# Kernel optimization log

Measured on AMD Instinct MI355X. Metric: run time of the kernel, lower is better.

Reference implementation:

```python
import jax, jax.numpy as jnp
import numpy as np
import math

D_MODEL = 1024
N_HEADS = 16
D_KV = 64
INNER = N_HEADS * D_KV
D_FF = 4096
NUM_BUCKETS = 32
MAX_DIST = 128
EPS = 1e-6
B, S = 2, 1024


def _t5_layernorm(x, w):
    # T5 RMSNorm: no mean subtraction, no bias
    var = jnp.mean(x * x, axis=-1, keepdims=True)
    return x * jax.lax.rsqrt(var + EPS) * w


def _relative_position_bucket(relative_position):
    # bidirectional (encoder) variant of T5 bucketing
    num_buckets = NUM_BUCKETS // 2
    rel_buckets = (relative_position > 0).astype(jnp.int32) * num_buckets
    rp = jnp.abs(relative_position)
    max_exact = num_buckets // 2
    is_small = rp < max_exact
    rp_large = max_exact + (
        jnp.log(rp.astype(jnp.float32) / max_exact)
        / math.log(MAX_DIST / max_exact)
        * (num_buckets - max_exact)
    ).astype(jnp.int32)
    rp_large = jnp.minimum(rp_large, num_buckets - 1)
    return rel_buckets + jnp.where(is_small, rp, rp_large)


def setup_inputs() -> dict:
    key = jax.random.key(0)
    ks = jax.random.split(key, 8)
    sc = 0.02
    return {
        "hidden_states": jax.random.normal(ks[0], (B, S, D_MODEL), jnp.float32),
        "ln1_w": jnp.ones((D_MODEL,), jnp.float32),
        "wq": jax.random.normal(ks[1], (INNER, D_MODEL), jnp.float32) * sc,
        "wk": jax.random.normal(ks[2], (INNER, D_MODEL), jnp.float32) * sc,
        "wv": jax.random.normal(ks[3], (INNER, D_MODEL), jnp.float32) * sc,
        "wo": jax.random.normal(ks[4], (D_MODEL, INNER), jnp.float32) * sc,
        "rel_bias": jax.random.normal(ks[5], (NUM_BUCKETS, N_HEADS), jnp.float32) * sc,
        "ln2_w": jnp.ones((D_MODEL,), jnp.float32),
        "wi": jax.random.normal(ks[6], (D_FF, D_MODEL), jnp.float32) * sc,
        "wo_ff": jax.random.normal(ks[7], (D_MODEL, D_FF), jnp.float32) * sc,
    }


def reference(hidden_states, ln1_w, wq, wk, wv, wo, rel_bias, ln2_w, wi, wo_ff):
    b, s, _ = hidden_states.shape
    # --- self-attention with relative position bias (T5: no 1/sqrt(d) scale) ---
    x = _t5_layernorm(hidden_states, ln1_w)
    q = (x @ wq.T).reshape(b, s, N_HEADS, D_KV).transpose(0, 2, 1, 3)  # [b,h,s,d]
    k = (x @ wk.T).reshape(b, s, N_HEADS, D_KV).transpose(0, 2, 1, 3)
    v = (x @ wv.T).reshape(b, s, N_HEADS, D_KV).transpose(0, 2, 1, 3)
    pos = jnp.arange(s)
    buckets = _relative_position_bucket(pos[None, :] - pos[:, None])  # [s,s]
    bias = rel_bias[buckets].transpose(2, 0, 1)[None]  # [1,h,s,s]
    scores = jnp.einsum('bhqd,bhkd->bhqk', q, k) + bias
    attn = jax.nn.softmax(scores, axis=-1)
    ctx = jnp.einsum('bhqk,bhkd->bhqd', attn, v)
    ctx = ctx.transpose(0, 2, 1, 3).reshape(b, s, INNER)
    h = hidden_states + ctx @ wo.T
    # --- FFN (ReLU dense) with pre-norm and residual ---
    y = _t5_layernorm(h, ln2_w)
    ff = jax.nn.relu(y @ wi.T) @ wo_ff.T
    return h + ff
```

## Files before the change

### kernel.cpp

```cpp
#include <hip/hip_runtime.h>
#include <hip/hip_bf16.h>
#include <math.h>


typedef __bf16 bf16_t;
typedef __attribute__((ext_vector_type(8))) __bf16 bf16x8;
typedef __attribute__((ext_vector_type(4))) __bf16 bf16x4;
typedef __attribute__((ext_vector_type(4))) float floatx4;

#define GLOBAL_AS(p) ((const __attribute__((address_space(1))) void*)(p))
#define LDS_AS(p)    ((__attribute__((address_space(3))) void*)(p))

__global__ __launch_bounds__(256) void convert_w_kernel(
    const float* __restrict__ wq, const float* __restrict__ wk,
    const float* __restrict__ wv, const float* __restrict__ wo,
    const float* __restrict__ wi, const float* __restrict__ woff,
    bf16_t* __restrict__ wqkv_b, bf16_t* __restrict__ wo_b,
    bf16_t* __restrict__ wi_b, bf16_t* __restrict__ woff_b) {
  size_t idx = ((size_t)blockIdx.x * 256 + threadIdx.x) * 8;
  const float* src;
  bf16_t* dst;
  size_t off;
  if (idx < 3145728) {
    size_t sec = idx >> 20;
    src = sec == 0 ? wq : (sec == 1 ? wk : wv);
    dst = wqkv_b + (sec << 20);
    off = idx & 1048575;
  } else if (idx < 4194304) {
    src = wo; dst = wo_b; off = idx - 3145728;
  } else if (idx < 8388608) {
    src = wi; dst = wi_b; off = idx - 4194304;
  } else {
    src = woff; dst = woff_b; off = idx - 8388608;
  }
  float4 a = *(const float4*)(src + off);
  float4 b = *(const float4*)(src + off + 4);
  bf16x8 o;
  o[0] = (bf16_t)a.x; o[1] = (bf16_t)a.y; o[2] = (bf16_t)a.z; o[3] = (bf16_t)a.w;
  o[4] = (bf16_t)b.x; o[5] = (bf16_t)b.y; o[6] = (bf16_t)b.z; o[7] = (bf16_t)b.w;
  *(bf16x8*)(dst + off) = o;
}

__global__ void bias_table_kernel(const float* __restrict__ rel_bias,
                                  float* __restrict__ table) {
  int idx = blockIdx.x * 256 + threadIdx.x;
  int h = idx >> 11;
  int dpos = idx & 2047;
  int delta = dpos - 1023;
  if (delta > 1023) delta = 1023;
  int side = (delta > 0) ? 16 : 0;
  int rp = (delta < 0) ? -delta : delta;
  int bucket;
  if (rp < 8) {
    bucket = side + rp;
  } else {
    float t3 = (logf((float)rp * 0.125f) / 2.7725887f) * 8.0f;
    int v = 8 + (int)t3;
    if (v > 15) v = 15;
    bucket = side + v;
  }
  table[idx] = rel_bias[bucket * 16 + h];
}

__global__ __launch_bounds__(256) void rmsnorm_kernel(
    const float* __restrict__ X, const float* __restrict__ w,
    bf16_t* __restrict__ Y) {
  const int D = 1024;
  int row = blockIdx.x;
  int t = threadIdx.x;
  float4 v = ((const float4*)(X + (size_t)row * D))[t];
  float f[4] = {v.x, v.y, v.z, v.w};
  float s = 0.f;
#pragma unroll
  for (int j = 0; j < 4; ++j) s += f[j] * f[j];
#pragma unroll
  for (int off = 32; off > 0; off >>= 1) s += __shfl_down(s, off);
  __shared__ float red[4];
  int lane = t & 63, wave = t >> 6;
  if (lane == 0) red[wave] = s;
  __syncthreads();
  float tot = red[0] + red[1] + red[2] + red[3];
  float scale = rsqrtf(tot * (1.0f / D) + 1e-6f);
  float4 wv4 = ((const float4*)w)[t];
  bf16x4 o;
  o[0] = (bf16_t)(f[0] * scale * wv4.x);
  o[1] = (bf16_t)(f[1] * scale * wv4.y);
  o[2] = (bf16_t)(f[2] * scale * wv4.z);
  o[3] = (bf16_t)(f[3] * scale * wv4.w);
  *(bf16x4*)(Y + (size_t)row * D + t * 4) = o;
}

template <int TBM, bool WF32, int OP>
__global__ __launch_bounds__(256, 2) void gemm_bt(
    const bf16_t* __restrict__ A, const void* __restrict__ W0,
    const void* __restrict__ W1, const void* __restrict__ W2,
    bf16_t* __restrict__ C, int M, int K_total, int klen, int N,
    int wsel_cols) {
  constexpr int MFRAG = TBM / 32;
  constexpr int ACH = TBM / 64;
  __shared__ bf16_t As[TBM * 32];
  __shared__ bf16_t Bs[128 * 32];

  const int tid = threadIdx.x;
  const int lane = tid & 63;
  const int wv = tid >> 6;
  const int wm = wv & 1;
  const int wn = wv >> 1;
  const int lr = lane & 15;
  const int lq = lane >> 4;

  const size_t row0 = (size_t)blockIdx.x * TBM;
  const size_t col0 = (size_t)blockIdx.y * 128;
  const int k0 = blockIdx.z * klen;

  const void* Ws = W0;
  size_t wc0 = col0;
  if ((int)col0 >= wsel_cols) {
    if ((int)col0 < 2 * wsel_cols) { Ws = W1; wc0 = col0 - wsel_cols; }
    else { Ws = W2; wc0 = col0 - 2 * (size_t)wsel_cols; }
  }

  const bf16_t* Abase = A + row0 * K_total;
  bf16_t* Cs = C + (size_t)blockIdx.z * M * N;

  floatx4 acc[MFRAG][4] = {};

  for (int kt = k0; kt < k0 + klen; kt += 32) {
#pragma unroll
    for (int i = 0; i < ACH; ++i) {
      int chunk = i * 256 + tid;
      int r = chunk >> 2;
      int kc = (chunk & 3) << 3;
      __builtin_amdgcn_global_load_lds(
          GLOBAL_AS(Abase + (size_t)r * K_total + kt + kc),
          LDS_AS(As + (size_t)(i * 256 + wv * 64) * 8), 16, 0, 0);
    }
    if constexpr (WF32) {
      const float* Wbase = (const float*)Ws + wc0 * K_total;
#pragma unroll
      for (int i = 0; i < 2; ++i) {
        int chunk = i * 256 + tid;
        int r = chunk >> 2;
        int kc = (chunk & 3) << 3;
        const float* p = Wbase + (size_t)r * K_total + kt + kc;
        float4 f0 = *(const float4*)p;
        float4 f1v = *(const float4*)(p + 4);
        bf16x8 o;
        o[0] = (bf16_t)f0.x; o[1] = (bf16_t)f0.y;
        o[2] = (bf16_t)f0.z; o[3] = (bf16_t)f0.w;
        o[4] = (bf16_t)f1v.x; o[5] = (bf16_t)f1v.y;
        o[6] = (bf16_t)f1v.z; o[7] = (bf16_t)f1v.w;
        *(bf16x8*)(Bs + chunk * 8) = o;
      }
    } else {
      const bf16_t* Wbase = (const bf16_t*)Ws + wc0 * K_total;
#pragma unroll
      for (int i = 0; i < 2; ++i) {
        int chunk = i * 256 + tid;
        int r = chunk >> 2;
        int kc = (chunk & 3) << 3;
        __builtin_amdgcn_global_load_lds(
            GLOBAL_AS(Wbase + (size_t)r * K_total + kt + kc),
            LDS_AS(Bs + (size_t)(i * 256 + wv * 64) * 8), 16, 0, 0);
      }
    }
    __syncthreads();

    bf16x8 af[MFRAG], bfr[4];
#pragma unroll
    for (int mi = 0; mi < MFRAG; ++mi)
      af[mi] = *(const bf16x8*)(As + (wm * (TBM / 2) + mi * 16 + lr) * 32 + lq * 8);
#pragma unroll
    for (int nj = 0; nj < 4; ++nj)
      bfr[nj] = *(const bf16x8*)(Bs + (wn * 64 + nj * 16 + lr) * 32 + lq * 8);

#pragma unroll
    for (int mi = 0; mi < MFRAG; ++mi)
#pragma unroll
      for (int nj = 0; nj < 4; ++nj)
        acc[mi][nj] = __builtin_amdgcn_mfma_f32_16x16x32_bf16(
            af[mi], bfr[nj], acc[mi][nj], 0, 0, 0);
    __syncthreads();
  }

#pragma unroll
  for (int mi = 0; mi < MFRAG; ++mi) {
#pragma unroll
    for (int nj = 0; nj < 4; ++nj) {
      size_t r = row0 + wm * (TBM / 2) + mi * 16 + lq * 4;
      size_t c = col0 + wn * 64 + nj * 16 + lr;
#pragma unroll
      for (int t = 0; t < 4; ++t) {
        float v = acc[mi][nj][t];
        if (OP == 2) v = v > 0.f ? v : 0.f;
        Cs[(r + t) * N + c] = (bf16_t)v;
      }
    }
  }
}

__global__ __launch_bounds__(256) void transpose_v_kernel(
    const bf16_t* __restrict__ QKV, bf16_t* __restrict__ VT) {
  __shared__ bf16_t T[64 * 65];
  const int s0 = blockIdx.x * 64;
  const int h = blockIdx.y;
  const int b = blockIdx.z;
  const int tid = threadIdx.x;

  const bf16_t* Vh = QKV + ((size_t)b * 1024) * 3072 + 2048 + h * 64;
#pragma unroll
  for (int i = 0; i < 2; ++i) {
    int c = i * 256 + tid;
    int r = c >> 3;
    int d8 = (c & 7) * 8;
    bf16x8 v = *(const bf16x8*)(Vh + (size_t)(s0 + r) * 3072 + d8);
#pragma unroll
    for (int j = 0; j < 8; ++j) T[r * 65 + d8 + j] = v[j];
  }
  __syncthreads();

  bf16_t* Og = VT + ((size_t)b * 16 + h) * 64 * 1024;
#pragma unroll
  for (int i = 0; i < 2; ++i) {
    int c = i * 256 + tid;
    int d = c >> 3;
    int s8 = (c & 7) * 8;
    bf16x8 o;
#pragma unroll
    for (int j = 0; j < 8; ++j) o[j] = T[(s8 + j) * 65 + d];
    *(bf16x8*)(Og + (size_t)d * 1024 + s0 + s8) = o;
  }
}

__device__ __forceinline__ void attn_stage(const bf16_t* Kh, const bf16_t* Vg,
                                           int k0, bf16_t* Ksb, bf16_t* Vtb,
                                           int tid, int wv) {
  const int l16 = tid & 15;
  const int lo8 = ((tid & 63) >> 4) * 8;
#pragma unroll
  for (int i = 0; i < 2; ++i) {
    int bi = wv * 2 + i;
    int g = bi >> 1, c = bi & 1;
    __builtin_amdgcn_global_load_lds(
        GLOBAL_AS(Kh + (size_t)(k0 + g * 16 + l16) * 3072 + c * 32 + lo8),
        LDS_AS(Ksb + bi * 512), 16, 0, 0);
    __builtin_amdgcn_global_load_lds(
        GLOBAL_AS(Vg + (size_t)(g * 16 + l16) * 1024 + k0 + c * 32 + lo8),
        LDS_AS(Vtb + bi * 512), 16, 0, 0);
  }
}

__global__ __launch_bounds__(256) void attn_kernel(
    const bf16_t* __restrict__ QKV, const bf16_t* __restrict__ VT,
    const float* __restrict__ bias_table, bf16_t* __restrict__ O) {
  const int qt = blockIdx.x;
  const int h = blockIdx.y;
  const int b = blockIdx.z;
  const int tid = threadIdx.x;
  const int lane = tid & 63;
  const int wv = tid >> 6;
  const int lr = lane & 15;
  const int lq = lane >> 4;

  __shared__ bf16_t Ks[2][4096];
  __shared__ bf16_t Vt[2][4096];
  __shared__ bf16_t Ps[4][1024];

  const bf16_t* Qh = QKV + (size_t)b * 1024 * 3072 + h * 64;
  const bf16_t* Kh = Qh + 1024;
  const bf16_t* Vg = VT + ((size_t)b * 16 + h) * 64 * 1024;
  bf16_t* Oh = O + (size_t)b * 1024 * 1024 + h * 64;

  const int q0w = qt * 64 + wv * 16;
  const int myq = q0w + lr;

  bf16x8 qf[2];
#pragma unroll
  for (int c = 0; c < 2; ++c)
    qf[c] = *(const bf16x8*)(Qh + (size_t)(q0w + lr) * 3072 + c * 32 + lq * 8);

  float l_loc = 0.f;
  floatx4 o_acc[4];
#pragma unroll
  for (int i = 0; i < 4; ++i) o_acc[i] = (floatx4){0.f, 0.f, 0.f, 0.f};

  const float* btab = bias_table + h * 2048 + 1023 - myq;

  attn_stage(Kh, Vg, 0, Ks[0], Vt[0], tid, wv);
  __syncthreads();

  for (int kt = 0; kt < 16; ++kt) {
    const int k0 = kt * 64;
    if (kt < 15)
      attn_stage(Kh, Vg, k0 + 64, Ks[(kt + 1) & 1], Vt[(kt + 1) & 1], tid, wv);
    const bf16_t* Ksb = Ks[kt & 1];
    const bf16_t* Vtb = Vt[kt & 1];

    floatx4 s_acc[4];
#pragma unroll
    for (int g = 0; g < 4; ++g) {
      floatx4 a = (floatx4){0.f, 0.f, 0.f, 0.f};
#pragma unroll
      for (int c = 0; c < 2; ++c) {
        bf16x8 kf = *(const bf16x8*)(Ksb + (g * 2 + c) * 512 + lane * 8);
        a = __builtin_amdgcn_mfma_f32_16x16x32_bf16(kf, qf[c], a, 0, 0, 0);
      }
      s_acc[g] = a;
    }

#pragma unroll
    for (int g = 0; g < 4; ++g) {
      bf16x4 pb;
#pragma unroll
      for (int t = 0; t < 4; ++t) {
        int key = k0 + g * 16 + lq * 4 + t;
        float p = __expf(s_acc[g][t] + btab[key] - 32.0f);
        l_loc += p;
        pb[t] = (bf16_t)p;
      }
      int c = g >> 1;
      int dst = c * 512 + (((g & 1) * 2 + (lq >> 1)) * 16 + lr) * 8 + (lq & 1) * 4;
      *(bf16x4*)(&Ps[wv][dst]) = pb;
    }

    asm volatile("s_waitcnt lgkmcnt(0)" ::: "memory");

    bf16x8 pf[2];
#pragma unroll
    for (int c = 0; c < 2; ++c)
      pf[c] = *(const bf16x8*)(&Ps[wv][c * 512 + lane * 8]);

#pragma unroll
    for (int g = 0; g < 4; ++g) {
#pragma unroll
      for (int c = 0; c < 2; ++c) {
        bf16x8 vf = *(const bf16x8*)(Vtb + (g * 2 + c) * 512 + lane * 8);
        o_acc[g] = __builtin_amdgcn_mfma_f32_16x16x32_bf16(pf[c], vf, o_acc[g], 0, 0, 0);
      }
    }
    __syncthreads();
  }

  l_loc += __shfl_xor(l_loc, 16);
  l_loc += __shfl_xor(l_loc, 32);
  float inv = 1.f / l_loc;

  float invt[4];
#pragma unroll
  for (int t = 0; t < 4; ++t) invt[t] = __shfl(inv, lq * 4 + t);

#pragma unroll
  for (int g = 0; g < 4; ++g) {
#pragma unroll
    for (int t = 0; t < 4; ++t) {
      int qg = q0w + lq * 4 + t;
      int d = g * 16 + lr;
      Oh[(size_t)qg * 1024 + d] = (bf16_t)(o_acc[g][t] * invt[t]);
    }
  }
}

__global__ __launch_bounds__(256) void reduce_rms_kernel(
    const bf16_t* __restrict__ part, int splits, const float* __restrict__ hs,
    const float* __restrict__ ln2w, bf16_t* __restrict__ hbuf,
    bf16_t* __restrict__ y) {
  const size_t SLICE = (size_t)2048 * 1024;
  int tid = threadIdx.x;
  size_t i = ((size_t)blockIdx.x * 256 + tid) * 8;

  float s[8] = {};
  for (int sp = 0; sp < splits; ++sp) {
    bf16x8 p = *(const bf16x8*)(part + sp * SLICE + i);
#pragma unroll
    for (int j = 0; j < 8; ++j) s[j] += (float)p[j];
  }
  float4 a = *(const float4*)(hs + i);
  float4 b = *(const float4*)(hs + i + 4);
  s[0] += a.x; s[1] += a.y; s[2] += a.z; s[3] += a.w;
  s[4] += b.x; s[5] += b.y; s[6] += b.z; s[7] += b.w;

  bf16x8 hb;
#pragma unroll
  for (int j = 0; j < 8; ++j) hb[j] = (bf16_t)s[j];
  *(bf16x8*)(hbuf + i) = hb;

  float ss = 0.f;
#pragma unroll
  for (int j = 0; j < 8; ++j) ss += s[j] * s[j];
#pragma unroll
  for (int off = 32; off > 0; off >>= 1) ss += __shfl_down(ss, off);
  __shared__ float red[4];
  int wave = tid >> 6;
  if ((tid & 63) == 0) red[wave] = ss;
  __syncthreads();
  float rowss = (tid < 128) ? (red[0] + red[1]) : (red[2] + red[3]);
  float scale = rsqrtf(rowss * (1.f / 1024.f) + 1e-6f);

  int col = (int)(i & 1023);
  float4 w0 = *(const float4*)(ln2w + col);
  float4 w1 = *(const float4*)(ln2w + col + 4);
  bf16x8 o;
  o[0] = (bf16_t)(s[0] * scale * w0.x); o[1] = (bf16_t)(s[1] * scale * w0.y);
  o[2] = (bf16_t)(s[2] * scale * w0.z); o[3] = (bf16_t)(s[3] * scale * w0.w);
  o[4] = (bf16_t)(s[4] * scale * w1.x); o[5] = (bf16_t)(s[5] * scale * w1.y);
  o[6] = (bf16_t)(s[6] * scale * w1.z); o[7] = (bf16_t)(s[7] * scale * w1.w);
  *(bf16x8*)(y + i) = o;
}

__global__ __launch_bounds__(256) void reduce_out_kernel(
    const bf16_t* __restrict__ part, int splits,
    const bf16_t* __restrict__ res, float* __restrict__ out) {
  const size_t SLICE = (size_t)2048 * 1024;
  size_t i = ((size_t)blockIdx.x * 256 + threadIdx.x) * 8;
  float s[8] = {};
  for (int sp = 0; sp < splits; ++sp) {
    bf16x8 p = *(const bf16x8*)(part + sp * SLICE + i);
#pragma unroll
    for (int j = 0; j < 8; ++j) s[j] += (float)p[j];
  }
  bf16x8 r = *(const bf16x8*)(res + i);
#pragma unroll
  for (int j = 0; j < 8; ++j) s[j] += (float)r[j];
  float4 a, b;
  a.x = s[0]; a.y = s[1]; a.z = s[2]; a.w = s[3];
  b.x = s[4]; b.y = s[5]; b.z = s[6]; b.w = s[7];
  *(float4*)(out + i) = a;
  *(float4*)(out + i + 4) = b;
}

extern "C" void kernel_launch(void* const* d_in, const int* in_sizes, int n_in,
                              void* d_out, int out_size, void* d_ws,
                              size_t ws_size, hipStream_t stream) {
  const float* hs = (const float*)d_in[0];
  const float* ln1_w = (const float*)d_in[1];
  const float* wq = (const float*)d_in[2];
  const float* wk = (const float*)d_in[3];
  const float* wvv = (const float*)d_in[4];
  const float* wo = (const float*)d_in[5];
  const float* rel_bias = (const float*)d_in[6];
  const float* ln2_w = (const float*)d_in[7];
  const float* wi = (const float*)d_in[8];
  const float* wo_ff = (const float*)d_in[9];
  float* out = (float*)d_out;

  const int M = 2048, D = 1024, FF = 4096;
  const size_t SL = (size_t)M * D * 2;
  const size_t QKVB = (size_t)M * 3072 * 2;
  const size_t F1B = (size_t)M * FF * 2;
  const size_t BT = 16 * 2048 * 4;

  const size_t FULL_NEED = BT + 6291456 + 2097152 + 8388608 + 8388608 +
                           SL + QKVB + SL + SL + SL + F1B + SL + 4 * SL;
  const size_t COMPACT_NEED = BT + SL + QKVB + F1B;

  char* w = (char*)d_ws;
  dim3 gtv(16, 16, 2), ga(16, 16, 2);

  if (ws_size >= FULL_NEED) {
    float* btab = (float*)w;      w += BT;
    bf16_t* wqkv_b = (bf16_t*)w;  w += 6291456;
    bf16_t* wo_b = (bf16_t*)w;    w += 2097152;
    bf16_t* wi_b = (bf16_t*)w;    w += 8388608;
    bf16_t* woff_b = (bf16_t*)w;  w += 8388608;
    bf16_t* x = (bf16_t*)w;       w += SL;
    bf16_t* qkv = (bf16_t*)w;     w += QKVB;
    bf16_t* ctx = (bf16_t*)w;     w += SL;
    bf16_t* hbuf = (bf16_t*)w;    w += SL;
    bf16_t* y = (bf16_t*)w;       w += SL;
    bf16_t* f1 = (bf16_t*)w;      w += F1B;
    bf16_t* vtg = (bf16_t*)w;     w += SL;
    bf16_t* part = (bf16_t*)w;    w += 4 * SL;

    convert_w_kernel<<<6144, 256, 0, stream>>>(wq, wk, wvv, wo, wi, wo_ff,
                                               wqkv_b, wo_b, wi_b, woff_b);
    bias_table_kernel<<<128, 256, 0, stream>>>(rel_bias, btab);
    rmsnorm_kernel<<<M, 256, 0, stream>>>(hs, ln1_w, x);

    gemm_bt<128, false, 0><<<dim3(16, 24, 1), 256, 0, stream>>>(
        x, wqkv_b, wqkv_b, wqkv_b, qkv, M, D, D, 3072, 1 << 30);
    transpose_v_kernel<<<gtv, 256, 0, stream>>>(qkv, vtg);
    attn_kernel<<<ga, 256, 0, stream>>>(qkv, vtg, btab, ctx);

    gemm_bt<128, false, 0><<<dim3(16, 8, 4), 256, 0, stream>>>(
        ctx, wo_b, wo_b, wo_b, part, M, D, D / 4, D, 1 << 30);
    reduce_rms_kernel<<<1024, 256, 0, stream>>>(part, 4, hs, ln2_w, hbuf, y);

    gemm_bt<128, false, 2><<<dim3(16, 32, 1), 256, 0, stream>>>(
        y, wi_b, wi_b, wi_b, f1, M, D, D, FF, 1 << 30);

    gemm_bt<128, false, 0><<<dim3(16, 8, 4), 256, 0, stream>>>(
        f1, woff_b, woff_b, woff_b, part, M, FF, FF / 4, D, 1 << 30);
    reduce_out_kernel<<<1024, 256, 0, stream>>>(part, 4, hbuf, out);
  } else {
    if (ws_size < COMPACT_NEED) return;
    float* btab = (float*)w;  w += BT;
    char* Abuf = w;           w += SL;
    char* Bbuf = w;           w += QKVB;
    char* Fbuf = w;           w += F1B;
    bf16_t* x = (bf16_t*)Abuf;
    bf16_t* ctx = (bf16_t*)Abuf;
    bf16_t* hbuf = (bf16_t*)Abuf;
    bf16_t* qkv = (bf16_t*)Bbuf;
    bf16_t* part = (bf16_t*)Bbuf;
    bf16_t* y = (bf16_t*)(Bbuf + 2 * SL);
    bf16_t* vtg = (bf16_t*)Fbuf;
    bf16_t* f1 = (bf16_t*)Fbuf;

    bias_table_kernel<<<128, 256, 0, stream>>>(rel_bias, btab);
    rmsnorm_kernel<<<M, 256, 0, stream>>>(hs, ln1_w, x);

    gemm_bt<64, true, 0><<<dim3(32, 24, 1), 256, 0, stream>>>(
        x, wq, wk, wvv, qkv, M, D, D, 3072, 1024);
    transpose_v_kernel<<<gtv, 256, 0, stream>>>(qkv, vtg);
    attn_kernel<<<ga, 256, 0, stream>>>(qkv, vtg, btab, ctx);

    gemm_bt<64, true, 0><<<dim3(32, 8, 2), 256, 0, stream>>>(
        ctx, wo, wo, wo, part, M, D, D / 2, D, 1 << 30);
    reduce_rms_kernel<<<1024, 256, 0, stream>>>(part, 2, hs, ln2_w, hbuf, y);

    gemm_bt<64, true, 2><<<dim3(32, 32, 1), 256, 0, stream>>>(
        y, wi, wi, wi, f1, M, D, D, FF, 1 << 30);

    gemm_bt<64, true, 0><<<dim3(32, 8, 2), 256, 0, stream>>>(
        f1, wo_ff, wo_ff, wo_ff, part, M, FF, FF / 2, D, 1 << 30);
    reduce_out_kernel<<<1024, 256, 0, stream>>>(part, 2, hbuf, out);
  }
}
```

Baseline: 247.8 us.

## Double GEMM K-tile to 64 with XOR-swizzled LDS and XCD-aware block remap

The GEMM K-step grows from 32 to 64, so each iteration loads twice as much data and performs two MFMA sub-steps per barrier pair, halving barrier and loop overhead. LDS chunks are stored with an XOR swizzle on the 16-byte column index to avoid bank conflicts on fragment reads. Block indices are also remapped so blocks that land on the same XCD share column tiles, for better L2 reuse. LDS use per block doubles, which may hurt occupancy, and the remap assumes gridDim.y is divisible by 8.

```diff
diff --git a/kernel.cpp b/kernel.cpp
--- a/kernel.cpp
+++ b/kernel.cpp
@@ -97,9 +97,8 @@
     bf16_t* __restrict__ C, int M, int K_total, int klen, int N,
     int wsel_cols) {
   constexpr int MFRAG = TBM / 32;
-  constexpr int ACH = TBM / 64;
-  __shared__ bf16_t As[TBM * 32];
-  __shared__ bf16_t Bs[128 * 32];
+  __shared__ bf16_t As[TBM * 64];
+  __shared__ bf16_t Bs[128 * 64];
 
   const int tid = threadIdx.x;
   const int lane = tid & 63;
@@ -109,8 +108,18 @@
   const int lr = lane & 15;
   const int lq = lane >> 4;
 
-  const size_t row0 = (size_t)blockIdx.x * TBM;
-  const size_t col0 = (size_t)blockIdx.y * 128;
+  int bx = blockIdx.x, by = blockIdx.y;
+  {
+    int gx = gridDim.x, gy = gridDim.y;
+    int lid = by * gx + bx;
+    int xcd = lid & 7, slot = lid >> 3;
+    int per = gy >> 3;
+    by = xcd * per + slot % per;
+    bx = slot / per;
+  }
+
+  const size_t row0 = (size_t)bx * TBM;
+  const size_t col0 = (size_t)by * 128;
   const int k0 = blockIdx.z * klen;
 
   const void* Ws = W0;
@@ -125,12 +134,12 @@
 
   floatx4 acc[MFRAG][4] = {};
 
-  for (int kt = k0; kt < k0 + klen; kt += 32) {
-#pragma unroll
-    for (int i = 0; i < ACH; ++i) {
+  for (int kt = k0; kt < k0 + klen; kt += 64) {
+#pragma unroll
+    for (int i = 0; i < TBM / 32; ++i) {
       int chunk = i * 256 + tid;
-      int r = chunk >> 2;
-      int kc = (chunk & 3) << 3;
+      int r = chunk >> 3;
+      int kc = ((chunk & 7) ^ (r & 7)) << 3;
       __builtin_amdgcn_global_load_lds(
           GLOBAL_AS(Abase + (size_t)r * K_total + kt + kc),
           LDS_AS(As + (size_t)(i * 256 + wv * 64) * 8), 16, 0, 0);
@@ -138,10 +147,10 @@
     if constexpr (WF32) {
       const float* Wbase = (const float*)Ws + wc0 * K_total;
 #pragma unroll
-      for (int i = 0; i < 2; ++i) {
+      for (int i = 0; i < 4; ++i) {
         int chunk = i * 256 + tid;
-        int r = chunk >> 2;
-        int kc = (chunk & 3) << 3;
+        int r = chunk >> 3;
+        int kc = ((chunk & 7) ^ (r & 7)) << 3;
         const float* p = Wbase + (size_t)r * K_total + kt + kc;
         float4 f0 = *(const float4*)p;
         float4 f1v = *(const float4*)(p + 4);
@@ -155,10 +164,10 @@
     } else {
       const bf16_t* Wbase = (const bf16_t*)Ws + wc0 * K_total;
 #pragma unroll
-      for (int i = 0; i < 2; ++i) {
+      for (int i = 0; i < 4; ++i) {
         int chunk = i * 256 + tid;
-        int r = chunk >> 2;
-        int kc = (chunk & 3) << 3;
+        int r = chunk >> 3;
+        int kc = ((chunk & 7) ^ (r & 7)) << 3;
         __builtin_amdgcn_global_load_lds(
             GLOBAL_AS(Wbase + (size_t)r * K_total + kt + kc),
             LDS_AS(Bs + (size_t)(i * 256 + wv * 64) * 8), 16, 0, 0);
@@ -166,20 +175,28 @@
     }
     __syncthreads();
 
-    bf16x8 af[MFRAG], bfr[4];
-#pragma unroll
-    for (int mi = 0; mi < MFRAG; ++mi)
-      af[mi] = *(const bf16x8*)(As + (wm * (TBM / 2) + mi * 16 + lr) * 32 + lq * 8);
-#pragma unroll
-    for (int nj = 0; nj < 4; ++nj)
-      bfr[nj] = *(const bf16x8*)(Bs + (wn * 64 + nj * 16 + lr) * 32 + lq * 8);
-
-#pragma unroll
-    for (int mi = 0; mi < MFRAG; ++mi)
-#pragma unroll
-      for (int nj = 0; nj < 4; ++nj)
-        acc[mi][nj] = __builtin_amdgcn_mfma_f32_16x16x32_bf16(
-            af[mi], bfr[nj], acc[mi][nj], 0, 0, 0);
+#pragma unroll
+    for (int c = 0; c < 2; ++c) {
+      bf16x8 af[MFRAG], bfr[4];
+#pragma unroll
+      for (int mi = 0; mi < MFRAG; ++mi) {
+        int rr = wm * (TBM / 2) + mi * 16 + lr;
+        int c8p = (c * 4 + lq) ^ (rr & 7);
+        af[mi] = *(const bf16x8*)(As + rr * 64 + c8p * 8);
+      }
+#pragma unroll
+      for (int nj = 0; nj < 4; ++nj) {
+        int rr = wn * 64 + nj * 16 + lr;
+        int c8p = (c * 4 + lq) ^ (rr & 7);
+        bfr[nj] = *(const bf16x8*)(Bs + rr * 64 + c8p * 8);
+      }
+#pragma unroll
+      for (int mi = 0; mi < MFRAG; ++mi)
+#pragma unroll
+        for (int nj = 0; nj < 4; ++nj)
+          acc[mi][nj] = __builtin_amdgcn_mfma_f32_16x16x32_bf16(
+              af[mi], bfr[nj], acc[mi][nj], 0, 0, 0);
+    }
     __syncthreads();
   }
 
```

After: 236.8 us. -4.4%, faster.
